# Performance work log

Hardware: AMD Instinct MI355X
Metric: run time of the kernel (lower is better)

## Reference

```python
import jax, jax.numpy as jnp
import numpy as np

B, LQ, LK, D, DV = 8, 2048, 2048, 128, 128


def setup_inputs() -> dict:
    key = jax.random.key(0)
    ks = jax.random.split(key, 6)
    return {
        "query": jax.random.normal(ks[0], (B, LQ, D), dtype=jnp.float32),
        "key": jax.random.normal(ks[1], (B, LK, D), dtype=jnp.float32),
        "value": jax.random.normal(ks[2], (B, LK, DV), dtype=jnp.float32),
        "Wq": jax.random.normal(ks[3], (D, D), dtype=jnp.float32) * 0.08,
        "Wk": jax.random.normal(ks[4], (D, D), dtype=jnp.float32) * 0.08,
        "Wv": jax.random.normal(ks[5], (DV, DV), dtype=jnp.float32) * 0.08,
        "attention_mask": jnp.ones((B, 1, LK), dtype=jnp.int32),
    }


def reference(query, key, value, Wq, Wk, Wv, attention_mask):
    # Linear projections (right-multiplication, as in `x @ W`)
    q = query @ Wq          # [B, lq, n_ed]
    k = key @ Wk            # [B, lk, n_ed]
    v = value @ Wv          # [B, lk, n_ev]
    scale = 1.0 / np.sqrt(q.shape[-1])
    scores = jnp.einsum("bqd,bkd->bqk", q, k) * scale  # [B, lq, lk]
    # additive mask: 0 where attend, -inf where mask==0 (broadcasts)
    mask_vals = jnp.where(attention_mask == 0, -jnp.inf, 0.0).astype(scores.dtype)
    scores = scores + mask_vals
    attn = jax.nn.softmax(scores, axis=-1)
    return attn @ v         # [B, lq, n_ev]
```

## Files before the change

kernel.cpp:

```cpp
#include <hip/hip_runtime.h>
#include <hip/hip_bf16.h>

typedef unsigned short u16;
typedef unsigned int u32;
typedef __attribute__((ext_vector_type(8))) short s8v;
typedef __attribute__((ext_vector_type(4))) float f4v;
typedef __attribute__((ext_vector_type(16))) float f16v;

#define B_N 8
#define L_Q 2048
#define L_K 2048
#define DIM 128
#define KT  64
#define KSPLIT 4
#define KCHUNK (L_K / KSPLIT)
#define NIT (KCHUNK / KT)

__device__ __forceinline__ u16 f2bf(float f) {
  union { float f; unsigned u; } v; v.f = f;
  return (u16)((v.u + 0x7fffu + ((v.u >> 16) & 1u)) >> 16);
}
__device__ __forceinline__ float bf2f(u16 u) {
  union { u32 u; float f; } v; v.u = ((u32)u) << 16; return v.f;
}
__device__ __forceinline__ u32 packbf2(float a, float b) {
  union { __hip_bfloat162 h; u32 u; } v;
  v.h = __float22bfloat162_rn(make_float2(a, b));
  return v.u;
}
__device__ __forceinline__ void async16(const u16* g, u16* l) {
  __builtin_amdgcn_global_load_lds(
      (const __attribute__((address_space(1))) u32*)(const void*)g,
      (__attribute__((address_space(3))) u32*)(void*)l, 16, 0, 0);
}


__global__ __launch_bounds__(256) void wprep(
    const float* __restrict__ Wq, const float* __restrict__ Wk,
    const float* __restrict__ Wv, u16* __restrict__ wbuf) {
  const int which = blockIdx.x;
  const int tid = threadIdx.x;
  const float* W = (which == 0) ? Wq : (which == 1) ? Wk : Wv;
  const float wscale = (which == 0) ? (1.44269504089f / 11.3137084990f) : 1.0f;
  u16* dst = wbuf + which * 16384;
#pragma unroll
  for (int i = 0; i < 16; ++i) {
    int f4i = tid + i * 256;
    float4 w4 = *(const float4*)(W + f4i * 4);
    int k = f4i >> 5, col = (f4i & 31) * 4;
    int ks = k >> 5, qd = (k & 31) >> 3, j = k & 7;
    float wv4[4] = {w4.x, w4.y, w4.z, w4.w};
#pragma unroll
    for (int c = 0; c < 4; ++c) {
      int n = col + c;
      dst[(ks * 8 + (n >> 4)) * 512 + (qd * 16 + (n & 15)) * 8 + j] = f2bf(wv4[c] * wscale);
    }
  }
}

__global__ __launch_bounds__(256, 3) void proj_mfma(
    const float* __restrict__ query, const float* __restrict__ key,
    const float* __restrict__ value, const u16* __restrict__ wbuf,
    u16* __restrict__ qp, u16* __restrict__ kp, u16* __restrict__ vp) {
  __shared__ __align__(16) u16 Wf[16384];
  __shared__ __align__(16) u16 Fb[8192];
  const int tid = threadIdx.x;
  const int bi = blockIdx.x;
  const int which = bi >> 8;
  const int sub = bi & 255;
  const int b = sub & 7;
  const int rt = sub >> 3;
  const float* X = (which == 0) ? query : (which == 1) ? key : value;
  const u16* Wfg = wbuf + which * 16384;

  const int w = tid >> 6, lane = tid & 63;
  const int ln = lane & 15, quad = lane >> 4;

#pragma unroll
  for (int c = 0; c < 8; ++c) {
    int cg = w * 8 + c;
    async16(Wfg + (size_t)(cg * 64 + lane) * 8, Wf + cg * 512);
  }

  const int xrow = rt * 64 + w * 16 + ln;
  const float* Xr = X + ((size_t)b * L_Q + xrow) * DIM;

  s8v a[4];
#pragma unroll
  for (int ks = 0; ks < 4; ++ks) {
    float4 xa = *(const float4*)(Xr + ks * 32 + quad * 8);
    float4 xb = *(const float4*)(Xr + ks * 32 + quad * 8 + 4);
    union { u32 wd[4]; s8v v; } t;
    t.wd[0] = packbf2(xa.x, xa.y);
    t.wd[1] = packbf2(xa.z, xa.w);
    t.wd[2] = packbf2(xb.x, xb.y);
    t.wd[3] = packbf2(xb.z, xb.w);
    a[ks] = t.v;
  }
  __syncthreads();

  f4v acc[8];
#pragma unroll
  for (int i = 0; i < 8; ++i) acc[i] = (f4v){0.f, 0.f, 0.f, 0.f};
#pragma unroll
  for (int ks = 0; ks < 4; ++ks)
#pragma unroll
    for (int nt = 0; nt < 8; ++nt) {
      s8v bw = *(const s8v*)(Wf + (ks * 8 + nt) * 512 + lane * 8);
      acc[nt] = __builtin_amdgcn_mfma_f32_16x16x32_bf16(a[ks], bw, acc[nt], 0, 0, 0);
    }

  if (which < 2) {
#pragma unroll
    for (int nt = 0; nt < 8; ++nt) {
      int base = ((w >> 1) * 8 + nt) * 512 + ((ln >> 3) * 32 + (w & 1) * 16 + quad * 4) * 8 + (ln & 7);
#pragma unroll
      for (int r = 0; r < 4; ++r) Fb[base + r * 8] = f2bf(acc[nt][r]);
    }
  } else {
#pragma unroll
    for (int nt = 0; nt < 8; ++nt) {
      int base = (w * 4 + (nt >> 1)) * 512 + ((quad >> 1) * 32 + (nt & 1) * 16 + ln) * 8 + (quad & 1) * 4;
      *(u32*)&Fb[base]     = packbf2(acc[nt][0], acc[nt][1]);
      *(u32*)&Fb[base + 2] = packbf2(acc[nt][2], acc[nt][3]);
    }
  }
  __syncthreads();

  u16* Y = ((which == 0) ? qp : (which == 1) ? kp : vp) + (size_t)(b * 32 + rt) * 8192;
#pragma unroll
  for (int r = 0; r < 4; ++r) {
    int c = tid + r * 256;
    *(s8v*)(Y + c * 8) = *(const s8v*)(Fb + c * 8);
  }
}

__global__ __launch_bounds__(256, 2) void flash_split(
    const u16* __restrict__ qp, const u16* __restrict__ kp,
    const u16* __restrict__ vp, const int* __restrict__ mask,
    u16* __restrict__ po, float* __restrict__ lbuf) {
  __shared__ __align__(16) u16 Kf[2][8192];
  __shared__ __align__(16) u16 Vf[2][8192];
  __shared__ float biasl[2][KT];

  const int tid = threadIdx.x;
  const int bi = blockIdx.x;
  const int b = bi & 7;
  const int rest = bi >> 3;
  const int p = rest & 3;
  const int qb = rest >> 2;
  const int w4 = tid >> 6;
  const int lane = tid & 63;
  const int qcol = lane & 31;
  const int H = lane >> 5;
  const bool Hb = (H != 0);

  const int* mb = mask + b * L_K;
  const int kt0 = p * NIT;

  auto stage = [&](int bufi, int kt_) {
    const u16* Ktile = kp + (size_t)(b * 32 + kt_) * 8192;
    const u16* Vtile = vp + (size_t)(b * 32 + kt_) * 8192;
#pragma unroll
    for (int c = 0; c < 4; ++c) {
      int f = w4 * 4 + c;
      async16(Ktile + (size_t)(f * 64 + lane) * 8, &Kf[bufi][f * 512]);
      async16(Vtile + (size_t)(f * 64 + lane) * 8, &Vf[bufi][f * 512]);
    }
  };

  const u16* Qt = qp + (size_t)(b * 64 + qb * 4 + w4) * 4096;
  s8v aq[8];
#pragma unroll
  for (int c = 0; c < 8; ++c) aq[c] = *(const s8v*)(Qt + c * 512 + lane * 8);

  f16v o[4];
#pragma unroll
  for (int i = 0; i < 4; ++i)
#pragma unroll
    for (int r = 0; r < 16; ++r) o[i][r] = 0.f;
  float lrow = 0.f;

  stage(0, kt0);
  int mv0 = mb[kt0 * KT + lane];
  bool ao_next = (__ballot(mv0 != 0) == ~0ull);
  if (!ao_next && tid < KT) biasl[0][tid] = (mv0 == 0) ? -__builtin_inff() : 0.f;
  __syncthreads();

  for (int it = 0; it < NIT; ++it) {
    const int cur = it & 1;
    const bool allones = ao_next;

    if (it + 1 < NIT) {
      stage(cur ^ 1, kt0 + it + 1);
      int mv = mb[(kt0 + it + 1) * KT + lane];
      ao_next = (__ballot(mv != 0) == ~0ull);
      if (!ao_next && tid < KT) biasl[cur ^ 1][tid] = (mv == 0) ? -__builtin_inff() : 0.f;
    }

    f16v s[2];
#pragma unroll
    for (int t = 0; t < 2; ++t)
#pragma unroll
      for (int r = 0; r < 16; ++r) s[t][r] = 0.f;
#pragma unroll
    for (int c = 0; c < 8; ++c) {
      s8v k0f = *(const s8v*)(&Kf[cur][c * 512] + lane * 8);
      s[0] = __builtin_amdgcn_mfma_f32_32x32x16_bf16(k0f, aq[c], s[0], 0, 0, 0);
      s8v k1f = *(const s8v*)(&Kf[cur][(8 + c) * 512] + lane * 8);
      s[1] = __builtin_amdgcn_mfma_f32_32x32x16_bf16(k1f, aq[c], s[1], 0, 0, 0);
    }
    if (!allones) {
#pragma unroll
      for (int t = 0; t < 2; ++t)
#pragma unroll
        for (int g = 0; g < 4; ++g) {
          float4 bt = *(const float4*)&biasl[cur][t * 32 + g * 8 + 4 * H];
          s[t][g * 4 + 0] += bt.x; s[t][g * 4 + 1] += bt.y;
          s[t][g * 4 + 2] += bt.z; s[t][g * 4 + 3] += bt.w;
        }
    }

    float rs = 0.f;
#pragma unroll
    for (int t = 0; t < 2; ++t)
#pragma unroll
      for (int r = 0; r < 16; ++r) {
        s[t][r] = __builtin_amdgcn_exp2f(s[t][r]);
        rs += s[t][r];
      }
    rs += __shfl_xor(rs, 32, 64);
    lrow += rs;

    u32 plo[2][4], phi[2][4];
#pragma unroll
    for (int t = 0; t < 2; ++t)
#pragma unroll
      for (int g = 0; g < 4; ++g) {
        plo[t][g] = packbf2(s[t][g * 4 + 0], s[t][g * 4 + 1]);
        phi[t][g] = packbf2(s[t][g * 4 + 2], s[t][g * 4 + 3]);
      }

#pragma unroll
    for (int kc = 0; kc < 4; ++kc) {
      const int t = kc >> 1, gl = (kc & 1) * 2;
      u32 a_lo0 = plo[t][gl], a_hi0 = phi[t][gl];
      u32 a_lo1 = plo[t][gl + 1], a_hi1 = phi[t][gl + 1];
      u32 snd_lo = Hb ? a_lo0 : a_lo1;
      u32 snd_hi = Hb ? a_hi0 : a_hi1;
      u32 r_lo = (u32)__shfl_xor((int)snd_lo, 32, 64);
      u32 r_hi = (u32)__shfl_xor((int)snd_hi, 32, 64);
      union { u32 wd[4]; s8v v; } pa;
      pa.wd[0] = Hb ? r_lo : a_lo0;
      pa.wd[1] = Hb ? r_hi : a_hi0;
      pa.wd[2] = Hb ? a_lo1 : r_lo;
      pa.wd[3] = Hb ? a_hi1 : r_hi;
#pragma unroll
      for (int ntv = 0; ntv < 4; ++ntv) {
        s8v bv = *(const s8v*)(&Vf[cur][(kc * 4 + ntv) * 512] + lane * 8);
        o[ntv] = __builtin_amdgcn_mfma_f32_32x32x16_bf16(pa.v, bv, o[ntv], 0, 0, 0);
      }
    }
    __syncthreads();
  }

  const size_t gidx = ((size_t)((p * 8 + b) * 16 + qb) * 4 + w4);
  u16* pw = po + gidx * 4096 + (size_t)lane * 16;
#pragma unroll
  for (int ntv = 0; ntv < 4; ++ntv) {
    union { u32 wd[4]; s8v v; } h1, h2;
#pragma unroll
    for (int j = 0; j < 4; ++j) {
      h1.wd[j] = packbf2(o[ntv][2 * j], o[ntv][2 * j + 1]);
      h2.wd[j] = packbf2(o[ntv][8 + 2 * j], o[ntv][9 + 2 * j]);
    }
    *(s8v*)(pw + ntv * 1024) = h1.v;
    *(s8v*)(pw + ntv * 1024 + 8) = h2.v;
  }
  if (H == 0) lbuf[gidx * 32 + qcol] = lrow;
}

__global__ __launch_bounds__(256) void combine(
    const u16* __restrict__ po, const float* __restrict__ lbuf,
    float* __restrict__ out) {
  __shared__ float shL[32];
  const int tid = threadIdx.x;
  const int bi = blockIdx.x;
  const int b = bi & 7;
  const int qb = (bi >> 3) & 15;
  const int w4 = bi >> 7;
  const int wv = tid >> 6;
  const int lane = tid & 63;
  const int qcol = lane & 31;
  const int H = lane >> 5;

  float acc[16];
#pragma unroll
  for (int r = 0; r < 16; ++r) acc[r] = 0.f;
#pragma unroll
  for (int p = 0; p < KSPLIT; ++p) {
    const u16* src = po + ((size_t)((p * 8 + b) * 16 + qb) * 4 + w4) * 4096 + (size_t)(wv * 64 + lane) * 16;
    s8v v1 = *(const s8v*)src;
    s8v v2 = *(const s8v*)(src + 8);
#pragma unroll
    for (int r = 0; r < 8; ++r) {
      acc[r] += bf2f((u16)v1[r]);
      acc[8 + r] += bf2f((u16)v2[r]);
    }
  }
  if (tid < 32) {
    float L = 0.f;
#pragma unroll
    for (int p = 0; p < KSPLIT; ++p)
      L += lbuf[((size_t)((p * 8 + b) * 16 + qb) * 4 + w4) * 32 + tid];
    shL[tid] = 1.0f / L;
  }
  __syncthreads();
#pragma unroll
  for (int reg = 0; reg < 16; ++reg) {
    int qloc = (reg & 3) + 8 * (reg >> 2) + 4 * H;
    size_t q = (size_t)b * L_Q + qb * 128 + w4 * 32 + qloc;
    out[q * DIM + wv * 32 + qcol] = acc[reg] * shL[qloc];
  }
}

extern "C" void kernel_launch(void* const* d_in, const int* in_sizes, int n_in,
                              void* d_out, int out_size, void* d_ws, size_t ws_size,
                              hipStream_t stream) {
  const float* query = (const float*)d_in[0];
  const float* key   = (const float*)d_in[1];
  const float* value = (const float*)d_in[2];
  const float* Wq    = (const float*)d_in[3];
  const float* Wk    = (const float*)d_in[4];
  const float* Wv    = (const float*)d_in[5];
  const int*   mask  = (const int*)d_in[6];
  float* out = (float*)d_out;

  u16* qp = (u16*)d_ws;
  u16* kp = qp + (size_t)B_N * L_Q * DIM;
  u16* vp = kp + (size_t)B_N * L_K * DIM;
  u16* po = vp + (size_t)B_N * DIM * L_K;
  float* lbuf = (float*)(po + (size_t)B_N * L_Q * KSPLIT * DIM);
  u16* wbuf = (u16*)(lbuf + (size_t)B_N * L_Q * KSPLIT);

  hipLaunchKernelGGL(wprep, dim3(3), dim3(256), 0, stream, Wq, Wk, Wv, wbuf);
  hipLaunchKernelGGL(proj_mfma, dim3(768), dim3(256), 0, stream,
                     query, key, value, wbuf, qp, kp, vp);
  hipLaunchKernelGGL(flash_split, dim3(512), dim3(256), 0, stream,
                     qp, kp, vp, mask, po, lbuf);
  hipLaunchKernelGGL(combine, dim3(512), dim3(256), 0, stream,
                     po, lbuf, out);
}
```

Baseline: 119.4 us.

## Fuse all stages into one cooperative persistent kernel with grid syncs

Merges weight prep, projection, split-K flash attention and combine into a single cooperative kernel of 512 blocks separated by grid.sync(), falling back to four separate launches when cooperative launch is unavailable. To fit the shared 32KB LDS budget, the flash loop now uses 32-key tiles with a 16-iteration double buffer. Warps are split between K and V staging, and the mask is read from global memory instead of an LDS bias table. The projection writes directly to global without an LDS transpose. This removes launch gaps and overhead, but adds grid-wide barrier cost, halves MFMA work per iteration, and makes projection output stores uncoalesced.

```diff
diff --git a/kernel.cpp b/kernel.cpp
--- a/kernel.cpp
+++ b/kernel.cpp
@@ -1,5 +1,8 @@
 #include <hip/hip_runtime.h>
 #include <hip/hip_bf16.h>
+#include <hip/hip_cooperative_groups.h>
+
+namespace cg = cooperative_groups;
 
 typedef unsigned short u16;
 typedef unsigned int u32;
@@ -11,10 +14,8 @@
 #define L_Q 2048
 #define L_K 2048
 #define DIM 128
-#define KT  64
 #define KSPLIT 4
-#define KCHUNK (L_K / KSPLIT)
-#define NIT (KCHUNK / KT)
+#define NHALF 16
 
 __device__ __forceinline__ u16 f2bf(float f) {
   union { float f; unsigned u; } v; v.f = f;
@@ -35,67 +36,58 @@
 }
 
 
-__global__ __launch_bounds__(256) void wprep(
-    const float* __restrict__ Wq, const float* __restrict__ Wk,
+__device__ __forceinline__ void wprep_dev(
+    int g, const float* __restrict__ Wq, const float* __restrict__ Wk,
     const float* __restrict__ Wv, u16* __restrict__ wbuf) {
-  const int which = blockIdx.x;
-  const int tid = threadIdx.x;
+  if (g >= 3 * 4096) return;
+  int which = g >> 12, f4i = g & 4095;
   const float* W = (which == 0) ? Wq : (which == 1) ? Wk : Wv;
   const float wscale = (which == 0) ? (1.44269504089f / 11.3137084990f) : 1.0f;
   u16* dst = wbuf + which * 16384;
-#pragma unroll
-  for (int i = 0; i < 16; ++i) {
-    int f4i = tid + i * 256;
-    float4 w4 = *(const float4*)(W + f4i * 4);
-    int k = f4i >> 5, col = (f4i & 31) * 4;
-    int ks = k >> 5, qd = (k & 31) >> 3, j = k & 7;
-    float wv4[4] = {w4.x, w4.y, w4.z, w4.w};
-#pragma unroll
-    for (int c = 0; c < 4; ++c) {
-      int n = col + c;
-      dst[(ks * 8 + (n >> 4)) * 512 + (qd * 16 + (n & 15)) * 8 + j] = f2bf(wv4[c] * wscale);
-    }
-  }
-}
-
-__global__ __launch_bounds__(256, 3) void proj_mfma(
-    const float* __restrict__ query, const float* __restrict__ key,
-    const float* __restrict__ value, const u16* __restrict__ wbuf,
-    u16* __restrict__ qp, u16* __restrict__ kp, u16* __restrict__ vp) {
-  __shared__ __align__(16) u16 Wf[16384];
-  __shared__ __align__(16) u16 Fb[8192];
-  const int tid = threadIdx.x;
-  const int bi = blockIdx.x;
-  const int which = bi >> 8;
-  const int sub = bi & 255;
+  float4 w4 = *(const float4*)(W + f4i * 4);
+  int k = f4i >> 5, col = (f4i & 31) * 4;
+  int ks = k >> 5, qd = (k & 31) >> 3, j = k & 7;
+  float wv4[4] = {w4.x, w4.y, w4.z, w4.w};
+#pragma unroll
+  for (int c = 0; c < 4; ++c) {
+    int n = col + c;
+    dst[(ks * 8 + (n >> 4)) * 512 + (qd * 16 + (n & 15)) * 8 + j] = f2bf(wv4[c] * wscale);
+  }
+}
+
+__device__ __forceinline__ void proj_dev(
+    int t, int tid, u16* shm, const float* __restrict__ query,
+    const float* __restrict__ key, const float* __restrict__ value,
+    const u16* __restrict__ wbuf, u16* __restrict__ qp, u16* __restrict__ kp,
+    u16* __restrict__ vp) {
+  const int which = t >> 8;
+  const int sub = t & 255;
   const int b = sub & 7;
   const int rt = sub >> 3;
   const float* X = (which == 0) ? query : (which == 1) ? key : value;
   const u16* Wfg = wbuf + which * 16384;
-
   const int w = tid >> 6, lane = tid & 63;
   const int ln = lane & 15, quad = lane >> 4;
 
 #pragma unroll
   for (int c = 0; c < 8; ++c) {
-    int cg = w * 8 + c;
-    async16(Wfg + (size_t)(cg * 64 + lane) * 8, Wf + cg * 512);
+    int cg_ = w * 8 + c;
+    async16(Wfg + (size_t)(cg_ * 64 + lane) * 8, shm + cg_ * 512);
   }
 
   const int xrow = rt * 64 + w * 16 + ln;
   const float* Xr = X + ((size_t)b * L_Q + xrow) * DIM;
-
   s8v a[4];
 #pragma unroll
   for (int ks = 0; ks < 4; ++ks) {
     float4 xa = *(const float4*)(Xr + ks * 32 + quad * 8);
     float4 xb = *(const float4*)(Xr + ks * 32 + quad * 8 + 4);
-    union { u32 wd[4]; s8v v; } t;
-    t.wd[0] = packbf2(xa.x, xa.y);
-    t.wd[1] = packbf2(xa.z, xa.w);
-    t.wd[2] = packbf2(xb.x, xb.y);
-    t.wd[3] = packbf2(xb.z, xb.w);
-    a[ks] = t.v;
+    union { u32 wd[4]; s8v v; } tt;
+    tt.wd[0] = packbf2(xa.x, xa.y);
+    tt.wd[1] = packbf2(xa.z, xa.w);
+    tt.wd[2] = packbf2(xb.x, xb.y);
+    tt.wd[3] = packbf2(xb.z, xb.w);
+    a[ks] = tt.v;
   }
   __syncthreads();
 
@@ -106,45 +98,34 @@
   for (int ks = 0; ks < 4; ++ks)
 #pragma unroll
     for (int nt = 0; nt < 8; ++nt) {
-      s8v bw = *(const s8v*)(Wf + (ks * 8 + nt) * 512 + lane * 8);
+      s8v bw = *(const s8v*)(shm + (ks * 8 + nt) * 512 + lane * 8);
       acc[nt] = __builtin_amdgcn_mfma_f32_16x16x32_bf16(a[ks], bw, acc[nt], 0, 0, 0);
     }
 
+  u16* Y = ((which == 0) ? qp : (which == 1) ? kp : vp) + (size_t)(b * 32 + rt) * 8192;
   if (which < 2) {
 #pragma unroll
     for (int nt = 0; nt < 8; ++nt) {
       int base = ((w >> 1) * 8 + nt) * 512 + ((ln >> 3) * 32 + (w & 1) * 16 + quad * 4) * 8 + (ln & 7);
 #pragma unroll
-      for (int r = 0; r < 4; ++r) Fb[base + r * 8] = f2bf(acc[nt][r]);
+      for (int r = 0; r < 4; ++r) Y[base + r * 8] = f2bf(acc[nt][r]);
     }
   } else {
 #pragma unroll
     for (int nt = 0; nt < 8; ++nt) {
       int base = (w * 4 + (nt >> 1)) * 512 + ((quad >> 1) * 32 + (nt & 1) * 16 + ln) * 8 + (quad & 1) * 4;
-      *(u32*)&Fb[base]     = packbf2(acc[nt][0], acc[nt][1]);
-      *(u32*)&Fb[base + 2] = packbf2(acc[nt][2], acc[nt][3]);
+      *(u32*)&Y[base]     = packbf2(acc[nt][0], acc[nt][1]);
+      *(u32*)&Y[base + 2] = packbf2(acc[nt][2], acc[nt][3]);
     }
   }
   __syncthreads();
-
-  u16* Y = ((which == 0) ? qp : (which == 1) ? kp : vp) + (size_t)(b * 32 + rt) * 8192;
-#pragma unroll
-  for (int r = 0; r < 4; ++r) {
-    int c = tid + r * 256;
-    *(s8v*)(Y + c * 8) = *(const s8v*)(Fb + c * 8);
-  }
-}
-
-__global__ __launch_bounds__(256, 2) void flash_split(
-    const u16* __restrict__ qp, const u16* __restrict__ kp,
-    const u16* __restrict__ vp, const int* __restrict__ mask,
-    u16* __restrict__ po, float* __restrict__ lbuf) {
-  __shared__ __align__(16) u16 Kf[2][8192];
-  __shared__ __align__(16) u16 Vf[2][8192];
-  __shared__ float biasl[2][KT];
-
-  const int tid = threadIdx.x;
-  const int bi = blockIdx.x;
+}
+
+__device__ __forceinline__ void flash_dev(
+    int bi, int tid, u16* shm, const u16* __restrict__ qp,
+    const u16* __restrict__ kp, const u16* __restrict__ vp,
+    const int* __restrict__ mask, u16* __restrict__ po,
+    float* __restrict__ lbuf) {
   const int b = bi & 7;
   const int rest = bi >> 3;
   const int p = rest & 3;
@@ -154,20 +135,8 @@
   const int qcol = lane & 31;
   const int H = lane >> 5;
   const bool Hb = (H != 0);
-
   const int* mb = mask + b * L_K;
-  const int kt0 = p * NIT;
-
-  auto stage = [&](int bufi, int kt_) {
-    const u16* Ktile = kp + (size_t)(b * 32 + kt_) * 8192;
-    const u16* Vtile = vp + (size_t)(b * 32 + kt_) * 8192;
-#pragma unroll
-    for (int c = 0; c < 4; ++c) {
-      int f = w4 * 4 + c;
-      async16(Ktile + (size_t)(f * 64 + lane) * 8, &Kf[bufi][f * 512]);
-      async16(Vtile + (size_t)(f * 64 + lane) * 8, &Vf[bufi][f * 512]);
-    }
-  };
+  const int hm0 = p * NHALF;
 
   const u16* Qt = qp + (size_t)(b * 64 + qb * 4 + w4) * 4096;
   s8v aq[8];
@@ -181,71 +150,78 @@
     for (int r = 0; r < 16; ++r) o[i][r] = 0.f;
   float lrow = 0.f;
 
-  stage(0, kt0);
-  int mv0 = mb[kt0 * KT + lane];
+  auto stage = [&](int bufi, int hm) {
+    const size_t off = (size_t)(b * 32 + (hm >> 1)) * 8192 + (hm & 1) * 4096;
+    if (w4 < 2) {
+#pragma unroll
+      for (int c = 0; c < 4; ++c) {
+        int f = w4 * 4 + c;
+        async16(kp + off + (size_t)(f * 64 + lane) * 8, shm + bufi * 4096 + f * 512);
+      }
+    } else {
+#pragma unroll
+      for (int c = 0; c < 4; ++c) {
+        int f = (w4 - 2) * 4 + c;
+        async16(vp + off + (size_t)(f * 64 + lane) * 8, shm + 8192 + bufi * 4096 + f * 512);
+      }
+    }
+  };
+
+  stage(0, hm0);
+  int mv0 = mb[hm0 * 32 + (tid & 31)];
   bool ao_next = (__ballot(mv0 != 0) == ~0ull);
-  if (!ao_next && tid < KT) biasl[0][tid] = (mv0 == 0) ? -__builtin_inff() : 0.f;
   __syncthreads();
 
-  for (int it = 0; it < NIT; ++it) {
+  for (int it = 0; it < NHALF; ++it) {
     const int cur = it & 1;
     const bool allones = ao_next;
-
-    if (it + 1 < NIT) {
-      stage(cur ^ 1, kt0 + it + 1);
-      int mv = mb[(kt0 + it + 1) * KT + lane];
+    const int k0 = (hm0 + it) * 32;
+    const u16* Kb = shm + cur * 4096;
+    const u16* Vb = shm + 8192 + cur * 4096;
+
+    if (it + 1 < NHALF) {
+      stage(cur ^ 1, hm0 + it + 1);
+      int mv = mb[(hm0 + it + 1) * 32 + (tid & 31)];
       ao_next = (__ballot(mv != 0) == ~0ull);
-      if (!ao_next && tid < KT) biasl[cur ^ 1][tid] = (mv == 0) ? -__builtin_inff() : 0.f;
-    }
-
-    f16v s[2];
-#pragma unroll
-    for (int t = 0; t < 2; ++t)
-#pragma unroll
-      for (int r = 0; r < 16; ++r) s[t][r] = 0.f;
+    }
+
+    f16v s;
+#pragma unroll
+    for (int r = 0; r < 16; ++r) s[r] = 0.f;
 #pragma unroll
     for (int c = 0; c < 8; ++c) {
-      s8v k0f = *(const s8v*)(&Kf[cur][c * 512] + lane * 8);
-      s[0] = __builtin_amdgcn_mfma_f32_32x32x16_bf16(k0f, aq[c], s[0], 0, 0, 0);
-      s8v k1f = *(const s8v*)(&Kf[cur][(8 + c) * 512] + lane * 8);
-      s[1] = __builtin_amdgcn_mfma_f32_32x32x16_bf16(k1f, aq[c], s[1], 0, 0, 0);
+      s8v bk = *(const s8v*)(Kb + c * 512 + lane * 8);
+      s = __builtin_amdgcn_mfma_f32_32x32x16_bf16(bk, aq[c], s, 0, 0, 0);
     }
     if (!allones) {
 #pragma unroll
-      for (int t = 0; t < 2; ++t)
-#pragma unroll
-        for (int g = 0; g < 4; ++g) {
-          float4 bt = *(const float4*)&biasl[cur][t * 32 + g * 8 + 4 * H];
-          s[t][g * 4 + 0] += bt.x; s[t][g * 4 + 1] += bt.y;
-          s[t][g * 4 + 2] += bt.z; s[t][g * 4 + 3] += bt.w;
-        }
+      for (int g = 0; g < 4; ++g)
+#pragma unroll
+        for (int i = 0; i < 4; ++i)
+          if (mb[k0 + g * 8 + 4 * H + i] == 0) s[g * 4 + i] = -__builtin_inff();
     }
 
     float rs = 0.f;
 #pragma unroll
-    for (int t = 0; t < 2; ++t)
-#pragma unroll
-      for (int r = 0; r < 16; ++r) {
-        s[t][r] = __builtin_amdgcn_exp2f(s[t][r]);
-        rs += s[t][r];
-      }
+    for (int r = 0; r < 16; ++r) {
+      s[r] = __builtin_amdgcn_exp2f(s[r]);
+      rs += s[r];
+    }
     rs += __shfl_xor(rs, 32, 64);
     lrow += rs;
 
-    u32 plo[2][4], phi[2][4];
-#pragma unroll
-    for (int t = 0; t < 2; ++t)
-#pragma unroll
-      for (int g = 0; g < 4; ++g) {
-        plo[t][g] = packbf2(s[t][g * 4 + 0], s[t][g * 4 + 1]);
-        phi[t][g] = packbf2(s[t][g * 4 + 2], s[t][g * 4 + 3]);
-      }
-
-#pragma unroll
-    for (int kc = 0; kc < 4; ++kc) {
-      const int t = kc >> 1, gl = (kc & 1) * 2;
-      u32 a_lo0 = plo[t][gl], a_hi0 = phi[t][gl];
-      u32 a_lo1 = plo[t][gl + 1], a_hi1 = phi[t][gl + 1];
+    u32 plo[4], phi[4];
+#pragma unroll
+    for (int g = 0; g < 4; ++g) {
+      plo[g] = packbf2(s[g * 4 + 0], s[g * 4 + 1]);
+      phi[g] = packbf2(s[g * 4 + 2], s[g * 4 + 3]);
+    }
+
+#pragma unroll
+    for (int kc = 0; kc < 2; ++kc) {
+      const int gl = kc * 2;
+      u32 a_lo0 = plo[gl], a_hi0 = phi[gl];
+      u32 a_lo1 = plo[gl + 1], a_hi1 = phi[gl + 1];
       u32 snd_lo = Hb ? a_lo0 : a_lo1;
       u32 snd_hi = Hb ? a_hi0 : a_hi1;
       u32 r_lo = (u32)__shfl_xor((int)snd_lo, 32, 64);
@@ -257,7 +233,7 @@
       pa.wd[3] = Hb ? a_hi1 : r_hi;
 #pragma unroll
       for (int ntv = 0; ntv < 4; ++ntv) {
-        s8v bv = *(const s8v*)(&Vf[cur][(kc * 4 + ntv) * 512] + lane * 8);
+        s8v bv = *(const s8v*)(Vb + (kc * 4 + ntv) * 512 + lane * 8);
         o[ntv] = __builtin_amdgcn_mfma_f32_32x32x16_bf16(pa.v, bv, o[ntv], 0, 0, 0);
       }
     }
@@ -280,12 +256,10 @@
   if (H == 0) lbuf[gidx * 32 + qcol] = lrow;
 }
 
-__global__ __launch_bounds__(256) void combine(
-    const u16* __restrict__ po, const float* __restrict__ lbuf,
-    float* __restrict__ out) {
-  __shared__ float shL[32];
-  const int tid = threadIdx.x;
-  const int bi = blockIdx.x;
+__device__ __forceinline__ void combine_dev(
+    int bi, int tid, u16* shm, const u16* __restrict__ po,
+    const float* __restrict__ lbuf, float* __restrict__ out) {
+  float* shL = (float*)shm;
   const int b = bi & 7;
   const int qb = (bi >> 3) & 15;
   const int w4 = bi >> 7;
@@ -322,6 +296,54 @@
     size_t q = (size_t)b * L_Q + qb * 128 + w4 * 32 + qloc;
     out[q * DIM + wv * 32 + qcol] = acc[reg] * shL[qloc];
   }
+}
+
+__global__ __launch_bounds__(256, 2) void fused(
+    const float* __restrict__ query, const float* __restrict__ key,
+    const float* __restrict__ value, const float* __restrict__ Wq,
+    const float* __restrict__ Wk, const float* __restrict__ Wv,
+    const int* __restrict__ mask, u16* __restrict__ qp, u16* __restrict__ kp,
+    u16* __restrict__ vp, u16* __restrict__ wbuf, u16* __restrict__ po,
+    float* __restrict__ lbuf, float* __restrict__ out) {
+  __shared__ __align__(16) u16 shm[16384];
+  cg::grid_group grid = cg::this_grid();
+  const int tid = threadIdx.x;
+  const int bi = blockIdx.x;
+
+  wprep_dev(bi * 256 + tid, Wq, Wk, Wv, wbuf);
+  grid.sync();
+  for (int t = bi; t < 768; t += 512)
+    proj_dev(t, tid, shm, query, key, value, wbuf, qp, kp, vp);
+  grid.sync();
+  flash_dev(bi, tid, shm, qp, kp, vp, mask, po, lbuf);
+  grid.sync();
+  combine_dev(bi, tid, shm, po, lbuf, out);
+}
+
+__global__ __launch_bounds__(256) void wprep_k(
+    const float* __restrict__ Wq, const float* __restrict__ Wk,
+    const float* __restrict__ Wv, u16* __restrict__ wbuf) {
+  wprep_dev(blockIdx.x * 256 + threadIdx.x, Wq, Wk, Wv, wbuf);
+}
+__global__ __launch_bounds__(256, 3) void proj_k(
+    const float* __restrict__ query, const float* __restrict__ key,
+    const float* __restrict__ value, const u16* __restrict__ wbuf,
+    u16* __restrict__ qp, u16* __restrict__ kp, u16* __restrict__ vp) {
+  __shared__ __align__(16) u16 shm[16384];
+  proj_dev(blockIdx.x, threadIdx.x, shm, query, key, value, wbuf, qp, kp, vp);
+}
+__global__ __launch_bounds__(256, 2) void flash_k(
+    const u16* __restrict__ qp, const u16* __restrict__ kp,
+    const u16* __restrict__ vp, const int* __restrict__ mask,
+    u16* __restrict__ po, float* __restrict__ lbuf) {
+  __shared__ __align__(16) u16 shm[16384];
+  flash_dev(blockIdx.x, threadIdx.x, shm, qp, kp, vp, mask, po, lbuf);
+}
+__global__ __launch_bounds__(256) void combine_k(
+    const u16* __restrict__ po, const float* __restrict__ lbuf,
+    float* __restrict__ out) {
+  __shared__ __align__(16) u16 shm[64];
+  combine_dev(blockIdx.x, threadIdx.x, shm, po, lbuf, out);
 }
 
 extern "C" void kernel_launch(void* const* d_in, const int* in_sizes, int n_in,
@@ -343,11 +365,24 @@
   float* lbuf = (float*)(po + (size_t)B_N * L_Q * KSPLIT * DIM);
   u16* wbuf = (u16*)(lbuf + (size_t)B_N * L_Q * KSPLIT);
 
-  hipLaunchKernelGGL(wprep, dim3(3), dim3(256), 0, stream, Wq, Wk, Wv, wbuf);
-  hipLaunchKernelGGL(proj_mfma, dim3(768), dim3(256), 0, stream,
+  int nb = 0;
+  hipError_t oe = hipOccupancyMaxActiveBlocksPerMultiprocessor(
+      &nb, (const void*)fused, 256, 0);
+  if (oe == hipSuccess && nb >= 2) {
+    void* args[] = {(void*)&query, (void*)&key, (void*)&value, (void*)&Wq,
+                    (void*)&Wk,    (void*)&Wv,  (void*)&mask,  (void*)&qp,
+                    (void*)&kp,    (void*)&vp,  (void*)&wbuf,  (void*)&po,
+                    (void*)&lbuf,  (void*)&out};
+    hipError_t le = hipLaunchCooperativeKernel((void*)fused, dim3(512),
+                                               dim3(256), args, 0, stream);
+    if (le == hipSuccess) return;
+  }
+
+  hipLaunchKernelGGL(wprep_k, dim3(48), dim3(256), 0, stream, Wq, Wk, Wv, wbuf);
+  hipLaunchKernelGGL(proj_k, dim3(768), dim3(256), 0, stream,
                      query, key, value, wbuf, qp, kp, vp);
-  hipLaunchKernelGGL(flash_split, dim3(512), dim3(256), 0, stream,
+  hipLaunchKernelGGL(flash_k, dim3(512), dim3(256), 0, stream,
                      qp, kp, vp, mask, po, lbuf);
-  hipLaunchKernelGGL(combine, dim3(512), dim3(256), 0, stream,
+  hipLaunchKernelGGL(combine_k, dim3(512), dim3(256), 0, stream,
                      po, lbuf, out);
 }
```

After: 115.5 us. 3.3% less time.
